# Kernel optimization log

Measured on AMD Instinct MI355X. Metric: run time of the kernel, lower is better.

## Reference

```python
import jax, jax.numpy as jnp
import numpy as np

DIM = 4096
N_HEADS = 32
N_KV = 8
HEAD_DIM = DIM // N_HEADS  # 128
R = N_HEADS // N_KV        # 4 query heads per kv head
B, T = 2, 2048


def setup_inputs() -> dict:
    key = jax.random.key(0)
    kx, kq, kkv, ko = jax.random.split(key, 4)
    scale = 0.02
    return {
        "x": jax.random.normal(kx, (B, T, DIM), dtype=jnp.float32),
        "Wq": jax.random.normal(kq, (DIM, DIM), dtype=jnp.float32) * scale,
        "Wkv": jax.random.normal(kkv, (2 * N_KV * HEAD_DIM, DIM), dtype=jnp.float32) * scale,
        "Wo": jax.random.normal(ko, (DIM, DIM), dtype=jnp.float32) * scale,
    }


def reference(x, Wq, Wkv, Wo):
    Bs, Ts, C = x.shape
    # projections (torch Linear: y = x @ W.T)
    q = (x @ Wq.T).reshape(Bs, Ts, N_HEADS, HEAD_DIM).transpose(0, 2, 1, 3)  # [B,H,T,hd]
    kv = x @ Wkv.T                                                            # [B,T,2*KV*hd]
    k, v = jnp.split(kv, 2, axis=-1)
    k = k.reshape(Bs, Ts, N_KV, HEAD_DIM).transpose(0, 2, 1, 3)  # [B,KV,T,hd]
    v = v.reshape(Bs, Ts, N_KV, HEAD_DIM).transpose(0, 2, 1, 3)  # [B,KV,T,hd]
    # grouped query heads: head h = g*R + r matches repeat_interleave(R, dim=1)
    qg = q.reshape(Bs, N_KV, R, Ts, HEAD_DIM)                    # [B,KV,R,T,hd]
    inv_scale = 1.0 / np.sqrt(HEAD_DIM).astype(np.float32)
    scores = jnp.einsum("bgrtd,bgsd->bgrts", qg, k) * inv_scale  # [B,KV,R,T,T]
    causal = jnp.tril(jnp.ones((Ts, Ts), dtype=bool))
    scores = jnp.where(causal, scores, jnp.finfo(scores.dtype).min)
    attn = jax.nn.softmax(scores, axis=-1)
    o = jnp.einsum("bgrts,bgsd->bgrtd", attn, v)                 # [B,KV,R,T,hd]
    o = o.reshape(Bs, N_HEADS, Ts, HEAD_DIM).transpose(0, 2, 1, 3).reshape(Bs, Ts, C)
    return o @ Wo.T
```

## Files before the change

### kernel.cpp

```cpp
#include <hip/hip_runtime.h>
#include <hip/hip_bf16.h>
#include <cstdint>
#include <type_traits>

#define DIM    4096
#define NHEADS 32
#define NKVH   8
#define HD     128
#define BATCH  2
#define SEQ    2048
#define MROWS  (BATCH*SEQ)
#define NQKV   6144
#define KOFF   4096
#define VOFF   5120

typedef __attribute__((ext_vector_type(8))) __bf16 bf16x8;
typedef __attribute__((ext_vector_type(4))) __bf16 bf16x4;
typedef __attribute__((ext_vector_type(4))) float  f32x4;

#define QSCALE 0.1275174338f

__device__ __forceinline__ void gl_lds16(const __bf16* g, __bf16* l) {
    __builtin_amdgcn_global_load_lds(
        (const __attribute__((address_space(1))) void*)g,
        (__attribute__((address_space(3))) void*)l, 16, 0, 0);
}

__global__ void cast_f32_bf16(const float* __restrict__ s, __bf16* __restrict__ d, int n8) {
    int i = blockIdx.x * 256 + threadIdx.x;
    if (i >= n8) return;
    float4 a = ((const float4*)s)[2*i];
    float4 b = ((const float4*)s)[2*i+1];
    bf16x8 v;
    v[0]=(__bf16)a.x; v[1]=(__bf16)a.y; v[2]=(__bf16)a.z; v[3]=(__bf16)a.w;
    v[4]=(__bf16)b.x; v[5]=(__bf16)b.y; v[6]=(__bf16)b.z; v[7]=(__bf16)b.w;
    ((bf16x8*)d)[i] = v;
}

template<typename OutT>
__global__ __launch_bounds__(256)
void gemm_bt(const __bf16* __restrict__ A, const __bf16* __restrict__ Bm,
             OutT* __restrict__ C, int M, int N, int K,
             float scale, int scale_cols)
{
    __shared__ __bf16 As[128*64];
    __shared__ __bf16 Bs[128*64];
    const int tid  = threadIdx.x;
    const int lane = tid & 63;
    const int w    = tid >> 6;
    const int quad = lane >> 4;
    const int l16  = lane & 15;
    const int m0   = blockIdx.y * 128;
    const int n0   = blockIdx.x * 128;
    const int wm   = (w & 1) * 64;
    const int wn   = (w >> 1) * 64;

    const __bf16* Ab = A  + (size_t)m0 * K;
    const __bf16* Bb = Bm + (size_t)n0 * K;

    f32x4 acc[4][4] = {};

    for (int k0 = 0; k0 < K; k0 += 64) {
        __syncthreads();
        #pragma unroll
        for (int r = 0; r < 4; ++r) {
            int chunk = r*256 + tid;
            int row = chunk >> 3, c8 = chunk & 7;
            int c8s = c8 ^ (row & 7);
            gl_lds16(Ab + (size_t)row*K + k0 + c8s*8, As + chunk*8);
            gl_lds16(Bb + (size_t)row*K + k0 + c8s*8, Bs + chunk*8);
        }
        __syncthreads();
        #pragma unroll
        for (int t = 0; t < 2; ++t) {
            bf16x8 af[4], bfr[4];
            #pragma unroll
            for (int i = 0; i < 4; ++i) {
                int row = wm + i*16 + l16;
                int cc  = (t*4 + quad) ^ (row & 7);
                af[i] = *(const bf16x8*)(As + row*64 + cc*8);
            }
            #pragma unroll
            for (int j = 0; j < 4; ++j) {
                int row = wn + j*16 + l16;
                int cc  = (t*4 + quad) ^ (row & 7);
                bfr[j] = *(const bf16x8*)(Bs + row*64 + cc*8);
            }
            #pragma unroll
            for (int i = 0; i < 4; ++i)
                #pragma unroll
                for (int j = 0; j < 4; ++j)
                    acc[i][j] = __builtin_amdgcn_mfma_f32_16x16x32_bf16(af[i], bfr[j], acc[i][j], 0,0,0);
        }
    }

    #pragma unroll
    for (int i = 0; i < 4; ++i) {
        #pragma unroll
        for (int j = 0; j < 4; ++j) {
            int col = n0 + wn + j*16 + l16;
            float sc = (col < scale_cols) ? scale : 1.0f;
            #pragma unroll
            for (int r = 0; r < 4; ++r) {
                int row = m0 + wm + i*16 + quad*4 + r;
                float v = acc[i][j][r] * sc;
                if constexpr (std::is_same<OutT, float>::value)
                    C[(size_t)row * N + col] = v;
                else
                    C[(size_t)row * N + col] = (__bf16)v;
            }
        }
    }
}

__global__ void transpose_v(const __bf16* __restrict__ qkv, __bf16* __restrict__ vt) {
    int idx  = blockIdx.x * 256 + threadIdx.x;
    int s8   = idx & 255;
    int rest = idx >> 8;
    int d    = rest & (HD-1);
    int bg   = rest >> 7;
    int b    = bg >> 3;
    int g    = bg & 7;
    int s0   = s8 * 8;
    const __bf16* src = qkv + (size_t)(b*SEQ + s0)*NQKV + VOFF + g*HD + d;
    bf16x8 v;
    #pragma unroll
    for (int u = 0; u < 8; ++u) v[u] = src[(size_t)u*NQKV];
    *(bf16x8*)(vt + (size_t)rest*SEQ + s0) = v;
}

__global__ __launch_bounds__(256, 4)
void flash_attn(const __bf16* __restrict__ qkv, const __bf16* __restrict__ vt,
                __bf16* __restrict__ O)
{
    __shared__ __bf16 Ks[64*128];
    __shared__ __bf16 Vts[128*64];
    __shared__ __bf16 Ps[64*64];

    const int qt = (gridDim.x - 1) - blockIdx.x;
    const int bh = blockIdx.y;
    const int b  = bh >> 5;
    const int h  = bh & 31;
    const int g  = h >> 2;
    const int q0 = qt * 64;

    const int tid  = threadIdx.x;
    const int lane = tid & 63;
    const int w    = tid >> 6;
    const int quad = lane >> 4;
    const int l16  = lane & 15;
    const int psw  = (l16 & 7) << 1;

    const __bf16* Qb  = qkv + (size_t)(b*SEQ + q0)*NQKV + h*HD;
    const __bf16* Kb  = qkv + (size_t)(b*SEQ)*NQKV + KOFF + g*HD;
    const __bf16* Vtb = vt  + (size_t)((b*NKVH + g)*HD)*SEQ;

    bf16x8 qf[4];
    #pragma unroll
    for (int t = 0; t < 4; ++t)
        qf[t] = *(const bf16x8*)(Qb + (size_t)(w*16 + l16)*NQKV + t*32 + quad*8);

    f32x4 o_acc[8] = {};
    float m_i = -1e30f, l_i = 0.f;
    const int myrow = q0 + w*16 + l16;

    const int nkt = qt + 1;
    for (int kt = 0; kt < nkt; ++kt) {
        const int s0 = kt * 64;
        __syncthreads();
        #pragma unroll
        for (int r = 0; r < 4; ++r) {
            int c = r*256 + tid;
            { int row = c >> 4, c16 = c & 15;
              int c16s = c16 ^ (row & 7);
              gl_lds16(Kb + (size_t)(s0 + row)*NQKV + c16s*8, Ks + c*8); }
            { int dd = c >> 3, c8 = c & 7;
              int c8s = c8 ^ (dd & 7);
              gl_lds16(Vtb + (size_t)dd*SEQ + s0 + c8s*8, Vts + c*8); }
        }
        __syncthreads();

        f32x4 s_acc[4] = {};
        #pragma unroll
        for (int t = 0; t < 4; ++t) {
            #pragma unroll
            for (int j = 0; j < 4; ++j) {
                int row = j*16 + l16;
                int cc  = (t*4 + quad) ^ (row & 7);
                bf16x8 bk = *(const bf16x8*)(Ks + row*128 + cc*8);
                s_acc[j] = __builtin_amdgcn_mfma_f32_16x16x32_bf16(bk, qf[t], s_acc[j], 0,0,0);
            }
        }

        if (kt == nkt - 1) {
            #pragma unroll
            for (int j = 0; j < 4; ++j)
                #pragma unroll
                for (int r = 0; r < 4; ++r)
                    if (s0 + j*16 + quad*4 + r > myrow) s_acc[j][r] = -1e30f;
        }

        float pm = s_acc[0][0];
        #pragma unroll
        for (int j = 0; j < 4; ++j)
            #pragma unroll
            for (int r = 0; r < 4; ++r)
                pm = fmaxf(pm, s_acc[j][r]);
        pm = fmaxf(pm, __shfl_xor(pm, 16));
        pm = fmaxf(pm, __shfl_xor(pm, 32));
        float mnew  = fmaxf(m_i, pm);
        float alpha = exp2f(m_i - mnew);
        m_i = mnew;

        float psum = 0.f;
        #pragma unroll
        for (int j = 0; j < 4; ++j) {
            bf16x4 pv;
            #pragma unroll
            for (int r = 0; r < 4; ++r) {
                float p = exp2f(s_acc[j][r] - mnew);
                psum += p;
                pv[r] = (__bf16)p;
            }
            int cs = (j*4 + quad) ^ psw;
            *(bf16x4*)(Ps + (w*16 + l16)*64 + cs*4) = pv;
        }
        psum += __shfl_xor(psum, 16);
        psum += __shfl_xor(psum, 32);
        l_i = l_i*alpha + psum;

        float av[4];
        #pragma unroll
        for (int r = 0; r < 4; ++r) av[r] = __shfl(alpha, quad*4 + r);
        #pragma unroll
        for (int jt = 0; jt < 8; ++jt)
            #pragma unroll
            for (int r = 0; r < 4; ++r)
                o_acc[jt][r] *= av[r];

        #pragma unroll
        for (int t = 0; t < 2; ++t) {
            int cs = (t*8 + quad*2) ^ psw;
            bf16x8 ap = *(const bf16x8*)(Ps + (w*16 + l16)*64 + cs*4);
            #pragma unroll
            for (int jt = 0; jt < 8; ++jt) {
                int row = jt*16 + l16;
                int cc  = (t*4 + quad) ^ (row & 7);
                bf16x8 bv = *(const bf16x8*)(Vts + row*64 + cc*8);
                o_acc[jt] = __builtin_amdgcn_mfma_f32_16x16x32_bf16(ap, bv, o_acc[jt], 0,0,0);
            }
        }
    }

    float inv = 1.0f / l_i;
    float ivr[4];
    #pragma unroll
    for (int r = 0; r < 4; ++r) ivr[r] = __shfl(inv, quad*4 + r);
    #pragma unroll
    for (int jt = 0; jt < 8; ++jt) {
        #pragma unroll
        for (int r = 0; r < 4; ++r) {
            int row = q0 + w*16 + quad*4 + r;
            int col = h*HD + jt*16 + l16;
            O[(size_t)(b*SEQ + row)*DIM + col] = (__bf16)(o_acc[jt][r] * ivr[r]);
        }
    }
}

extern "C" void kernel_launch(void* const* d_in, const int* in_sizes, int n_in,
                              void* d_out, int out_size, void* d_ws, size_t ws_size,
                              hipStream_t stream) {
    const float* x   = (const float*)d_in[0];
    const float* Wq  = (const float*)d_in[1];
    const float* Wkv = (const float*)d_in[2];
    const float* Wo  = (const float*)d_in[3];

    const size_t OFF_XB   = 0;
    const size_t OFF_WQKV = 33554432;
    const size_t OFF_WO   = 83886080;
    const size_t OFF_QKV  = 117440512;
    const size_t OFF_VT   = 167772160;
    const size_t OFF_OB   = 176160768;
    const size_t NEEDED   = 209715200;
    if (ws_size < NEEDED) return;

    char* ws = (char*)d_ws;
    __bf16* xb   = (__bf16*)(ws + OFF_XB);
    __bf16* wqkv = (__bf16*)(ws + OFF_WQKV);
    __bf16* wo   = (__bf16*)(ws + OFF_WO);
    __bf16* qkv  = (__bf16*)(ws + OFF_QKV);
    __bf16* vt   = (__bf16*)(ws + OFF_VT);
    __bf16* ob   = (__bf16*)(ws + OFF_OB);

    cast_f32_bf16<<<16777216/8/256, 256, 0, stream>>>(x,   xb,              16777216/8);
    cast_f32_bf16<<<16777216/8/256, 256, 0, stream>>>(Wq,  wqkv,            16777216/8);
    cast_f32_bf16<<< 8388608/8/256, 256, 0, stream>>>(Wkv, wqkv + 16777216,  8388608/8);
    cast_f32_bf16<<<16777216/8/256, 256, 0, stream>>>(Wo,  wo,              16777216/8);

    gemm_bt<__bf16><<<dim3(NQKV/128, MROWS/128), 256, 0, stream>>>(
        xb, wqkv, qkv, MROWS, NQKV, DIM, QSCALE, DIM);

    transpose_v<<<524288/256, 256, 0, stream>>>(qkv, vt);

    flash_attn<<<dim3(SEQ/64, BATCH*NHEADS), 256, 0, stream>>>(qkv, vt, ob);

    gemm_bt<float><<<dim3(DIM/128, MROWS/128), 256, 0, stream>>>(
        ob, wo, (float*)d_out, MROWS, DIM, DIM, 1.0f, 0);
}
```

Baseline: 850.6 us.

## Process two 64-row query tiles per flash-attention block to reuse K/V loads

Measured after the change: 1.347 ms. 1.58x slower.

```diff
diff --git a/kernel.cpp b/kernel.cpp
--- a/kernel.cpp
+++ b/kernel.cpp
@@ -129,20 +129,20 @@
     *(bf16x8*)(vt + (size_t)rest*SEQ + s0) = v;
 }
 
-__global__ __launch_bounds__(256, 4)
+__global__ __launch_bounds__(256)
 void flash_attn(const __bf16* __restrict__ qkv, const __bf16* __restrict__ vt,
                 __bf16* __restrict__ O)
 {
     __shared__ __bf16 Ks[64*128];
     __shared__ __bf16 Vts[128*64];
-    __shared__ __bf16 Ps[64*64];
+    __shared__ __bf16 Ps[128*64];
 
     const int qt = (gridDim.x - 1) - blockIdx.x;
     const int bh = blockIdx.y;
     const int b  = bh >> 5;
     const int h  = bh & 31;
     const int g  = h >> 2;
-    const int q0 = qt * 64;
+    const int q0 = qt * 128;
 
     const int tid  = threadIdx.x;
     const int lane = tid & 63;
@@ -151,20 +151,24 @@
     const int l16  = lane & 15;
     const int psw  = (l16 & 7) << 1;
 
-    const __bf16* Qb  = qkv + (size_t)(b*SEQ + q0)*NQKV + h*HD;
+    const __bf16* QbA = qkv + (size_t)(b*SEQ + q0)*NQKV + h*HD;
+    const __bf16* QbB = QbA + (size_t)64*NQKV;
     const __bf16* Kb  = qkv + (size_t)(b*SEQ)*NQKV + KOFF + g*HD;
     const __bf16* Vtb = vt  + (size_t)((b*NKVH + g)*HD)*SEQ;
 
-    bf16x8 qf[4];
+    bf16x8 qfA[4], qfB[4];
     #pragma unroll
-    for (int t = 0; t < 4; ++t)
-        qf[t] = *(const bf16x8*)(Qb + (size_t)(w*16 + l16)*NQKV + t*32 + quad*8);
-
-    f32x4 o_acc[8] = {};
-    float m_i = -1e30f, l_i = 0.f;
-    const int myrow = q0 + w*16 + l16;
-
-    const int nkt = qt + 1;
+    for (int t = 0; t < 4; ++t) {
+        qfA[t] = *(const bf16x8*)(QbA + (size_t)(w*16 + l16)*NQKV + t*32 + quad*8);
+        qfB[t] = *(const bf16x8*)(QbB + (size_t)(w*16 + l16)*NQKV + t*32 + quad*8);
+    }
+
+    f32x4 oA[8] = {}, oB[8] = {};
+    float mA = -1e30f, lA = 0.f, mB = -1e30f, lB = 0.f;
+    const int rowA = q0 + w*16 + l16;
+    const int rowB = rowA + 64;
+
+    const int nkt = 2*qt + 2;
     for (int kt = 0; kt < nkt; ++kt) {
         const int s0 = kt * 64;
         __syncthreads();
@@ -180,90 +184,162 @@
         }
         __syncthreads();
 
-        f32x4 s_acc[4] = {};
-        #pragma unroll
-        for (int t = 0; t < 4; ++t) {
+        const bool actA = (kt <= 2*qt);
+
+        if (actA) {
+            f32x4 s_acc[4] = {};
+            #pragma unroll
+            for (int t = 0; t < 4; ++t)
+                #pragma unroll
+                for (int j = 0; j < 4; ++j) {
+                    int row = j*16 + l16;
+                    int cc  = (t*4 + quad) ^ (row & 7);
+                    bf16x8 bk = *(const bf16x8*)(Ks + row*128 + cc*8);
+                    s_acc[j] = __builtin_amdgcn_mfma_f32_16x16x32_bf16(bk, qfA[t], s_acc[j], 0,0,0);
+                }
+            if (kt == 2*qt) {
+                #pragma unroll
+                for (int j = 0; j < 4; ++j)
+                    #pragma unroll
+                    for (int r = 0; r < 4; ++r)
+                        if (s0 + j*16 + quad*4 + r > rowA) s_acc[j][r] = -1e30f;
+            }
+            float pm = s_acc[0][0];
+            #pragma unroll
+            for (int j = 0; j < 4; ++j)
+                #pragma unroll
+                for (int r = 0; r < 4; ++r)
+                    pm = fmaxf(pm, s_acc[j][r]);
+            pm = fmaxf(pm, __shfl_xor(pm, 16));
+            pm = fmaxf(pm, __shfl_xor(pm, 32));
+            float mnew  = fmaxf(mA, pm);
+            float alpha = exp2f(mA - mnew);
+            mA = mnew;
+            float psum = 0.f;
             #pragma unroll
             for (int j = 0; j < 4; ++j) {
-                int row = j*16 + l16;
-                int cc  = (t*4 + quad) ^ (row & 7);
-                bf16x8 bk = *(const bf16x8*)(Ks + row*128 + cc*8);
-                s_acc[j] = __builtin_amdgcn_mfma_f32_16x16x32_bf16(bk, qf[t], s_acc[j], 0,0,0);
-            }
-        }
-
-        if (kt == nkt - 1) {
+                bf16x4 pv;
+                #pragma unroll
+                for (int r = 0; r < 4; ++r) {
+                    float p = exp2f(s_acc[j][r] - mnew);
+                    psum += p;
+                    pv[r] = (__bf16)p;
+                }
+                int cs = (j*4 + quad) ^ psw;
+                *(bf16x4*)(Ps + (w*16 + l16)*64 + cs*4) = pv;
+            }
+            psum += __shfl_xor(psum, 16);
+            psum += __shfl_xor(psum, 32);
+            lA = lA*alpha + psum;
+            float av[4];
+            #pragma unroll
+            for (int r = 0; r < 4; ++r) av[r] = __shfl(alpha, quad*4 + r);
+            #pragma unroll
+            for (int jt = 0; jt < 8; ++jt)
+                #pragma unroll
+                for (int r = 0; r < 4; ++r)
+                    oA[jt][r] *= av[r];
+        }
+
+        {
+            f32x4 s_acc[4] = {};
+            #pragma unroll
+            for (int t = 0; t < 4; ++t)
+                #pragma unroll
+                for (int j = 0; j < 4; ++j) {
+                    int row = j*16 + l16;
+                    int cc  = (t*4 + quad) ^ (row & 7);
+                    bf16x8 bk = *(const bf16x8*)(Ks + row*128 + cc*8);
+                    s_acc[j] = __builtin_amdgcn_mfma_f32_16x16x32_bf16(bk, qfB[t], s_acc[j], 0,0,0);
+                }
+            if (kt == 2*qt + 1) {
+                #pragma unroll
+                for (int j = 0; j < 4; ++j)
+                    #pragma unroll
+                    for (int r = 0; r < 4; ++r)
+                        if (s0 + j*16 + quad*4 + r > rowB) s_acc[j][r] = -1e30f;
+            }
+            float pm = s_acc[0][0];
             #pragma unroll
             for (int j = 0; j < 4; ++j)
                 #pragma unroll
                 for (int r = 0; r < 4; ++r)
-                    if (s0 + j*16 + quad*4 + r > myrow) s_acc[j][r] = -1e30f;
-        }
-
-        float pm = s_acc[0][0];
-        #pragma unroll
-        for (int j = 0; j < 4; ++j)
-            #pragma unroll
-            for (int r = 0; r < 4; ++r)
-                pm = fmaxf(pm, s_acc[j][r]);
-        pm = fmaxf(pm, __shfl_xor(pm, 16));
-        pm = fmaxf(pm, __shfl_xor(pm, 32));
-        float mnew  = fmaxf(m_i, pm);
-        float alpha = exp2f(m_i - mnew);
-        m_i = mnew;
-
-        float psum = 0.f;
-        #pragma unroll
-        for (int j = 0; j < 4; ++j) {
-            bf16x4 pv;
-            #pragma unroll
-            for (int r = 0; r < 4; ++r) {
-                float p = exp2f(s_acc[j][r] - mnew);
-                psum += p;
-                pv[r] = (__bf16)p;
-            }
-            int cs = (j*4 + quad) ^ psw;
-            *(bf16x4*)(Ps + (w*16 + l16)*64 + cs*4) = pv;
-        }
-        psum += __shfl_xor(psum, 16);
-        psum += __shfl_xor(psum, 32);
-        l_i = l_i*alpha + psum;
-
-        float av[4];
-        #pragma unroll
-        for (int r = 0; r < 4; ++r) av[r] = __shfl(alpha, quad*4 + r);
-        #pragma unroll
-        for (int jt = 0; jt < 8; ++jt)
-            #pragma unroll
-            for (int r = 0; r < 4; ++r)
-                o_acc[jt][r] *= av[r];
+                    pm = fmaxf(pm, s_acc[j][r]);
+            pm = fmaxf(pm, __shfl_xor(pm, 16));
+            pm = fmaxf(pm, __shfl_xor(pm, 32));
+            float mnew  = fmaxf(mB, pm);
+            float alpha = exp2f(mB - mnew);
+            mB = mnew;
+            float psum = 0.f;
+            #pragma unroll
+            for (int j = 0; j < 4; ++j) {
+                bf16x4 pv;
+                #pragma unroll
+                for (int r = 0; r < 4; ++r) {
+                    float p = exp2f(s_acc[j][r] - mnew);
+                    psum += p;
+                    pv[r] = (__bf16)p;
+                }
+                int cs = (j*4 + quad) ^ psw;
+                *(bf16x4*)(Ps + (64 + w*16 + l16)*64 + cs*4) = pv;
+            }
+            psum += __shfl_xor(psum, 16);
+            psum += __shfl_xor(psum, 32);
+            lB = lB*alpha + psum;
+            float av[4];
+            #pragma unroll
+            for (int r = 0; r < 4; ++r) av[r] = __shfl(alpha, quad*4 + r);
+            #pragma unroll
+            for (int jt = 0; jt < 8; ++jt)
+                #pragma unroll
+                for (int r = 0; r < 4; ++r)
+                    oB[jt][r] *= av[r];
+        }
 
         #pragma unroll
         for (int t = 0; t < 2; ++t) {
             int cs = (t*8 + quad*2) ^ psw;
-            bf16x8 ap = *(const bf16x8*)(Ps + (w*16 + l16)*64 + cs*4);
+            bf16x8 apB = *(const bf16x8*)(Ps + (64 + w*16 + l16)*64 + cs*4);
+            bf16x8 apA;
+            if (actA) apA = *(const bf16x8*)(Ps + (w*16 + l16)*64 + cs*4);
             #pragma unroll
             for (int jt = 0; jt < 8; ++jt) {
                 int row = jt*16 + l16;
                 int cc  = (t*4 + quad) ^ (row & 7);
                 bf16x8 bv = *(const bf16x8*)(Vts + row*64 + cc*8);
-                o_acc[jt] = __builtin_amdgcn_mfma_f32_16x16x32_bf16(ap, bv, o_acc[jt], 0,0,0);
-            }
-        }
-    }
-
-    float inv = 1.0f / l_i;
-    float ivr[4];
-    #pragma unroll
-    for (int r = 0; r < 4; ++r) ivr[r] = __shfl(inv, quad*4 + r);
-    #pragma unroll
-    for (int jt = 0; jt < 8; ++jt) {
-        #pragma unroll
-        for (int r = 0; r < 4; ++r) {
-            int row = q0 + w*16 + quad*4 + r;
-            int col = h*HD + jt*16 + l16;
-            O[(size_t)(b*SEQ + row)*DIM + col] = (__bf16)(o_acc[jt][r] * ivr[r]);
-        }
+                if (actA) oA[jt] = __builtin_amdgcn_mfma_f32_16x16x32_bf16(apA, bv, oA[jt], 0,0,0);
+                oB[jt] = __builtin_amdgcn_mfma_f32_16x16x32_bf16(apB, bv, oB[jt], 0,0,0);
+            }
+        }
+    }
+
+    {
+        float inv = 1.0f / lA;
+        float ivr[4];
+        #pragma unroll
+        for (int r = 0; r < 4; ++r) ivr[r] = __shfl(inv, quad*4 + r);
+        #pragma unroll
+        for (int jt = 0; jt < 8; ++jt)
+            #pragma unroll
+            for (int r = 0; r < 4; ++r) {
+                int row = q0 + w*16 + quad*4 + r;
+                int col = h*HD + jt*16 + l16;
+                O[(size_t)(b*SEQ + row)*DIM + col] = (__bf16)(oA[jt][r] * ivr[r]);
+            }
+    }
+    {
+        float inv = 1.0f / lB;
+        float ivr[4];
+        #pragma unroll
+        for (int r = 0; r < 4; ++r) ivr[r] = __shfl(inv, quad*4 + r);
+        #pragma unroll
+        for (int jt = 0; jt < 8; ++jt)
+            #pragma unroll
+            for (int r = 0; r < 4; ++r) {
+                int row = q0 + 64 + w*16 + quad*4 + r;
+                int col = h*HD + jt*16 + l16;
+                O[(size_t)(b*SEQ + row)*DIM + col] = (__bf16)(oB[jt][r] * ivr[r]);
+            }
     }
 }
 
@@ -302,7 +378,7 @@
 
     transpose_v<<<524288/256, 256, 0, stream>>>(qkv, vt);
 
-    flash_attn<<<dim3(SEQ/64, BATCH*NHEADS), 256, 0, stream>>>(qkv, vt, ob);
+    flash_attn<<<dim3(SEQ/128, BATCH*NHEADS), 256, 0, stream>>>(qkv, vt, ob);
 
     gemm_bt<float><<<dim3(DIM/128, MROWS/128), 256, 0, stream>>>(
         ob, wo, (float*)d_out, MROWS, DIM, DIM, 1.0f, 0);
```
